# Performance work log

Hardware: AMD Instinct MI355X
Metric: run time of the kernel (lower is better)

The kernel has to match this reference:

```python
import jax, jax.numpy as jnp
import numpy as np

BLOCKS = 32
BLOCK_SIZE = 8
CONV_SHAPES = [(128, 96), (128, 128), (96, 128)] * 2  # per-block conv (out,in) list


def build_conv_meta():
    meta = []
    w_total = 0
    b_total = 0
    for _ in range(BLOCKS):
        for oc, ic in CONV_SHAPES:
            meta.append((oc, ic, w_total, b_total))
            w_total += oc * ic * 9
            b_total += oc
    return meta, w_total, b_total

CONV_META, W_TOTAL, B_TOTAL = build_conv_meta()


def build_program():
    ops = [[0, 0, 0, 0], [1, 0, 0, 0], [2, 0, 0, 0]]
    for blk in range(BLOCKS):
        ops.append([3, 0, 1, 2])  # SPLIT r0 -> (r1, r2)
        for rnd in range(2):
            ci = blk * 6 + rnd * 3
            ops += [
                [4, 3, 2, ci],      # r3 = conv(r2)        128<-96
                [5, 3, 3, 0],       # r3 = relu(r3)
                [4, 3, 3, ci + 1],  # r3 = conv(r3)        128<-128
                [5, 3, 3, 0],       # r3 = relu(r3)
                [4, 3, 3, ci + 2],  # r3 = conv(r3)        96<-128
                [6, 1, 1, 3],       # r1 = r1 + r3
                [9, 1, 2, 0],       # swap(r1, r2)  (Feistel)
            ]
        ops += [[7, 0, 1, 2],       # r0 = concat(r1, r2)
                [8, 0, 0, blk]]     # r0 = mix[blk] @ r0 (1x1 conv)
    return np.array(ops, dtype=np.int64)


def space_to_depth(x, blk):
    b, c, h, w = x.shape
    x = x.reshape(b, c, h // blk, blk, w // blk, blk)
    x = jnp.transpose(x, (0, 1, 3, 5, 2, 4))
    return x.reshape(b, c * blk * blk, h // blk, w // blk)


def conv3x3(x, w, b):
    y = jax.lax.conv_general_dilated(
        x, w, window_strides=(1, 1), padding=[(1, 1), (1, 1)],
        dimension_numbers=('NCHW', 'OIHW', 'NCHW'))
    return y + b[None, :, None, None]


def run_program(x, mu, sigma, w_flat, b_flat, m, perm, ops):
    regs = [x, None, None, None, None]
    for row in np.asarray(ops):
        op, a, b, c = (int(v) for v in row)
        if op == 0:  # AFFINE
            regs[a] = (regs[a] - mu[None, :, None, None]) / sigma[None, :, None, None]
        elif op == 1:  # PERM: gather along flattened HW per channel
            bs, ch, h, w = regs[a].shape
            v = regs[a].reshape(bs, ch, h * w)
            regs[a] = jnp.take_along_axis(v, perm[None], axis=2).reshape(bs, ch, h, w)
        elif op == 2:  # S2D
            regs[a] = space_to_depth(regs[a], BLOCK_SIZE)
        elif op == 3:  # SPLIT
            regs[b], regs[c] = jnp.split(regs[a], 2, axis=1)
        elif op == 4:  # CONV (weights sliced from flat buffer, static offsets)
            oc, ic, woff, boff = CONV_META[c]
            w = w_flat[woff:woff + oc * ic * 9].reshape(oc, ic, 3, 3)
            bb = b_flat[boff:boff + oc]
            regs[a] = conv3x3(regs[b], w, bb)
        elif op == 5:  # RELU
            regs[a] = jax.nn.relu(regs[b])
        elif op == 6:  # ADD
            regs[a] = regs[b] + regs[c]
        elif op == 7:  # CONCAT
            regs[a] = jnp.concatenate([regs[b], regs[c]], axis=1)
        elif op == 8:  # MIX: 1x1 conv with 192x192 orthogonal matrix
            regs[a] = jnp.einsum('oc,bchw->bohw', m[c], regs[b])
        elif op == 9:  # SWAP
            regs[a], regs[b] = regs[b], regs[a]
        else:
            raise ValueError('bad op')
    return regs[0]


def setup_inputs() -> dict:
    key = jax.random.key(0)
    k_x, k_w, k_b = jax.random.split(key, 3)
    rng = np.random.default_rng(0)

    x = jax.random.normal(k_x, (8, 3, 256, 256), dtype=jnp.float32)
    mu = jnp.full((3,), 0.45, dtype=jnp.float32)
    sigma = jnp.full((3,), 0.2, dtype=jnp.float32)
    # conv weights ~ He-ish scale so activations stay bounded across 64 Feistel rounds
    w_flat = jax.random.normal(k_w, (W_TOTAL,), dtype=jnp.float32) * 0.04
    b_flat = jax.random.normal(k_b, (B_TOTAL,), dtype=jnp.float32) * 0.01
    # orthogonal 192x192 mix matrices per block (as in nn.init.orthogonal_)
    ms = []
    for _ in range(BLOCKS):
        q, r = np.linalg.qr(rng.standard_normal((192, 192)))
        q = q * np.sign(np.diag(r))[None, :]
        ms.append(q.astype(np.float32))
    m = jnp.asarray(np.stack(ms))  # [BLOCKS,192,192]
    # per-channel spatial permutation on the 256x256 input
    perm = jnp.asarray(np.stack([rng.permutation(256 * 256) for _ in range(3)]).astype(np.int32))
    ops = build_program()  # static numpy tape
    return {'x': x, 'mu': mu, 'sigma': sigma, 'w_flat': w_flat, 'b_flat': b_flat,
            'm': m, 'perm': perm, 'ops': ops}


def reference(x, mu, sigma, w_flat, b_flat, m, perm, ops):
    return run_program(x, mu, sigma, w_flat, b_flat, m, perm, ops)
```

## Files before the change

### kernel.cpp

```cpp
#include <hip/hip_runtime.h>

typedef _Float16 f16;
typedef _Float16 f16x8 __attribute__((ext_vector_type(8)));
typedef _Float16 f16x4 __attribute__((ext_vector_type(4)));
typedef float    f32x4 __attribute__((ext_vector_type(4)));

#define TPB 256

__global__ __launch_bounds__(TPB) void prologue_k(
    const float* __restrict__ x, const float* __restrict__ mu,
    const float* __restrict__ sigma, const int* __restrict__ perm,
    f16* __restrict__ A0)
{
    int gid = blockIdx.x * TPB + threadIdx.x;
    if (gid >= 8192 * 192) return;
    int c = gid % 192;
    int p = gid / 192;
    int b  = p >> 10;
    int h2 = (p >> 5) & 31;
    int w2 = p & 31;
    int cc = c >> 6;
    int bh = (c >> 3) & 7;
    int bw = c & 7;
    int j   = (h2 * 8 + bh) * 256 + (w2 * 8 + bw);
    int src = perm[cc * 65536 + j];
    float v = (x[(b * 3 + cc) * 65536 + src] - mu[cc]) / sigma[cc];
    A0[gid] = (f16)v;
}

__global__ __launch_bounds__(TPB) void wconv_k(const float* __restrict__ wf,
                                               f16* __restrict__ wh)
{
    int c   = blockIdx.y;
    int idx = blockIdx.x * TPB + threadIdx.x;
    int s   = c % 6;
    int s3  = s % 3;
    int oc  = (s3 == 2) ? 96 : 128;
    int ic  = (s3 == 0) ? 96 : 128;
    int wo  = (s3 == 0 ? 0 : (s3 == 1 ? 110592 : 258048)) + (s >= 3 ? 368640 : 0);
    int ocic = oc * ic;
    int n    = ocic * 9;
    if (idx >= n) return;
    size_t base = (size_t)(c / 6) * 737280 + wo;
    int tap = idx / ocic;
    int r   = idx - tap * ocic;
    int o   = r / ic;
    int i   = r - o * ic;
    wh[base + idx] = (f16)wf[base + (size_t)o * ic * 9 + (size_t)i * 9 + tap];
}

__global__ __launch_bounds__(TPB) void mconv_k(const float* __restrict__ mf,
                                               f16* __restrict__ mh, int n)
{
    int i = blockIdx.x * TPB + threadIdx.x;
    if (i < n) mh[i] = (f16)mf[i];
}

__global__ __launch_bounds__(TPB) void bconv_k(const float* __restrict__ bf,
                                               float* __restrict__ bs, int n)
{
    int i = blockIdx.x * TPB + threadIdx.x;
    if (i < n) bs[i] = ldexpf(bf[i], -(i / 704));
}

template<int IC, int OC, int TAPS, bool RELU, bool ACCUM, bool OUT32>
__global__ __launch_bounds__(TPB) void conv_k(
    const f16* __restrict__ Xin, int ICS,
    const f16* __restrict__ W,  const float* __restrict__ bias,
    f16* __restrict__ Out, int OCS, float* __restrict__ Out32, float scale)
{
    constexpr int R    = 4;
    constexpr int NC8  = IC / 8;
    constexpr int PAD  = (TAPS == 9) ? 1 : 0;
    constexpr int ROWS = R + 2 * PAD;
    constexpr int WW   = 32 + 2 * PAD;

    extern __shared__ f16 lds[];
    f16* Alds = lds + ROWS * NC8 * WW * 8;

    const int tid  = threadIdx.x;
    const int tile = blockIdx.x;
    const int img  = tile >> 3;
    const int r0   = (tile & 7) * R;
    const int oc0  = blockIdx.y * 32;

    for (int i = tid; i < ROWS * WW * NC8; i += TPB) {
        int c8  = i % NC8;
        int rem = i / NC8;
        int wv  = rem % WW;
        int ri  = rem / WW;
        int row = r0 - PAD + ri;
        int wc  = wv - PAD;
        f16x8 v = {};
        if ((unsigned)row < 32u && (unsigned)wc < 32u) {
            int p = img * 1024 + row * 32 + wc;
            v = *(const f16x8*)&Xin[(size_t)p * ICS + c8 * 8];
        }
        *(f16x8*)&lds[((ri * NC8 + c8) * WW + wv) * 8] = v;
    }

    const int lane = tid & 63;
    const int wave = tid >> 6;
    const int lq   = lane >> 4;
    const int ln   = lane & 15;

    f32x4 acc[2][2] = {};

    for (int tap = 0; tap < TAPS; ++tap) {
        __syncthreads();
        for (int i = tid; i < 32 * NC8; i += TPB) {
            int o  = i & 31;
            int c8 = i >> 5;
            *(f16x8*)&Alds[(c8 * 32 + o) * 8] =
                *(const f16x8*)&W[((size_t)tap * OC + oc0 + o) * IC + c8 * 8];
        }
        __syncthreads();

        const int dy = (TAPS == 9) ? tap / 3 - 1 : 0;
        const int dx = (TAPS == 9) ? tap % 3 - 1 : 0;
        const int bb = ((wave + PAD + dy) * NC8 * WW + (ln + dx + PAD)) * 8;

#pragma unroll
        for (int kc = 0; kc < IC / 32; ++kc) {
            f16x8 a0 = *(const f16x8*)&Alds[((kc * 4 + lq) * 32 + ln) * 8];
            f16x8 a1 = *(const f16x8*)&Alds[((kc * 4 + lq) * 32 + 16 + ln) * 8];
            f16x8 b0 = *(const f16x8*)&lds[bb + (kc * 4 + lq) * WW * 8];
            f16x8 b1 = *(const f16x8*)&lds[bb + (kc * 4 + lq) * WW * 8 + 128];
            acc[0][0] = __builtin_amdgcn_mfma_f32_16x16x32_f16(a0, b0, acc[0][0], 0, 0, 0);
            acc[1][0] = __builtin_amdgcn_mfma_f32_16x16x32_f16(a1, b0, acc[1][0], 0, 0, 0);
            acc[0][1] = __builtin_amdgcn_mfma_f32_16x16x32_f16(a0, b1, acc[0][1], 0, 0, 0);
            acc[1][1] = __builtin_amdgcn_mfma_f32_16x16x32_f16(a1, b1, acc[1][1], 0, 0, 0);
        }
    }

    const int prow = r0 + wave;
#pragma unroll
    for (int mm = 0; mm < 2; ++mm) {
#pragma unroll
        for (int nn = 0; nn < 2; ++nn) {
            int oc = oc0 + mm * 16 + lq * 4;
            int p  = img * 1024 + prow * 32 + nn * 16 + ln;
            float b0 = 0.f, b1 = 0.f, b2 = 0.f, b3 = 0.f;
            if (TAPS == 9) {
                float4 bv = *(const float4*)&bias[oc];
                b0 = bv.x; b1 = bv.y; b2 = bv.z; b3 = bv.w;
            }
            float v0 = acc[mm][nn][0] * scale + b0;
            float v1 = acc[mm][nn][1] * scale + b1;
            float v2 = acc[mm][nn][2] * scale + b2;
            float v3 = acc[mm][nn][3] * scale + b3;
            if (RELU) {
                v0 = fmaxf(v0, 0.f); v1 = fmaxf(v1, 0.f);
                v2 = fmaxf(v2, 0.f); v3 = fmaxf(v3, 0.f);
            }
            if (OUT32) {
                size_t ob = (size_t)(img * 192 + oc) * 1024 + prow * 32 + nn * 16 + ln;
                Out32[ob]          = v0;
                Out32[ob + 1024]   = v1;
                Out32[ob + 2048]   = v2;
                Out32[ob + 3072]   = v3;
            } else {
                f16* op = &Out[(size_t)p * OCS + oc];
                if (ACCUM) {
                    f16x4 old = *(const f16x4*)op;
                    v0 += (float)old[0]; v1 += (float)old[1];
                    v2 += (float)old[2]; v3 += (float)old[3];
                }
                f16x4 hv;
                hv[0] = (f16)v0; hv[1] = (f16)v1; hv[2] = (f16)v2; hv[3] = (f16)v3;
                *(f16x4*)op = hv;
            }
        }
    }
}

extern "C" void kernel_launch(void* const* d_in, const int* in_sizes, int n_in,
                              void* d_out, int out_size, void* d_ws, size_t ws_size,
                              hipStream_t stream)
{
    const float* x     = (const float*)d_in[0];
    const float* mu    = (const float*)d_in[1];
    const float* sigma = (const float*)d_in[2];
    const float* wf    = (const float*)d_in[3];
    const float* bf    = (const float*)d_in[4];
    const float* mf    = (const float*)d_in[5];
    const int*   perm  = (const int*)d_in[6];
    float*       out   = (float*)d_out;

    char* ws = (char*)d_ws;
    f16*   WH = (f16*)(ws);
    f16*   MH = (f16*)(ws + 47185920);
    float* BS = (float*)(ws + 49545216);
    f16*   XA = (f16*)(ws + 49635328);
    f16*   XB = (f16*)(ws + 52781056);
    f16*   H1 = (f16*)(ws + 55926784);
    f16*   H2 = (f16*)(ws + 58023936);

    wconv_k<<<dim3(576, 192), TPB, 0, stream>>>(wf, WH);
    mconv_k<<<dim3(4608), TPB, 0, stream>>>(mf, MH, 1179648);
    bconv_k<<<dim3(88),   TPB, 0, stream>>>(bf, BS, 22528);
    prologue_k<<<dim3(6144), TPB, 0, stream>>>(x, mu, sigma, perm, XA);

    static const int wo6[6] = {0, 110592, 258048, 368640, 479232, 626688};
    static const int bo6[6] = {0, 128, 256, 352, 480, 608};

    constexpr int LDS96  = (6 * 12 * 34 * 8 + 96 * 32) * 2;
    constexpr int LDS128 = (6 * 16 * 34 * 8 + 128 * 32) * 2;
    constexpr int LDS192 = (4 * 24 * 32 * 8 + 192 * 32) * 2;

    f16* cur = XA;
    f16* nxt = XB;
    for (int blk = 0; blk < 32; ++blk) {
        int c = blk * 6;
        size_t w0 = (size_t)blk * 737280;
        size_t b0 = (size_t)blk * 704;
        conv_k<96, 128, 9, true,  false, false><<<dim3(64, 4), TPB, LDS96, stream>>>(
            cur + 96, 192, WH + w0 + wo6[0], BS + b0 + bo6[0], H1, 128, nullptr, 1.0f);
        conv_k<128, 128, 9, true,  false, false><<<dim3(64, 4), TPB, LDS128, stream>>>(
            H1, 128, WH + w0 + wo6[1], BS + b0 + bo6[1], H2, 128, nullptr, 1.0f);
        conv_k<128, 96, 9, false, true,  false><<<dim3(64, 3), TPB, LDS128, stream>>>(
            H2, 128, WH + w0 + wo6[2], BS + b0 + bo6[2], cur, 192, nullptr, 1.0f);
        conv_k<96, 128, 9, true,  false, false><<<dim3(64, 4), TPB, LDS96, stream>>>(
            cur, 192, WH + w0 + wo6[3], BS + b0 + bo6[3], H1, 128, nullptr, 1.0f);
        conv_k<128, 128, 9, true,  false, false><<<dim3(64, 4), TPB, LDS128, stream>>>(
            H1, 128, WH + w0 + wo6[4], BS + b0 + bo6[4], H2, 128, nullptr, 1.0f);
        conv_k<128, 96, 9, false, true,  false><<<dim3(64, 3), TPB, LDS128, stream>>>(
            H2, 128, WH + w0 + wo6[5], BS + b0 + bo6[5], cur + 96, 192, nullptr, 1.0f);
        if (blk < 31) {
            conv_k<192, 192, 1, false, false, false><<<dim3(64, 6), TPB, LDS192, stream>>>(
                cur, 192, MH + (size_t)blk * 36864, nullptr, nxt, 192, nullptr, 0.5f);
        } else {
            conv_k<192, 192, 1, false, false, true><<<dim3(64, 6), TPB, LDS192, stream>>>(
                cur, 192, MH + (size_t)blk * 36864, nullptr, nullptr, 192, out,
                2147483648.0f );
        }
        f16* t = cur; cur = nxt; nxt = t;
    }
}
```

Measured before the change: 3.036 ms.

## Replace per-layer launches with persistent kernel using per-image spin barriers

After: 3.718 ms. 1.22x slower.

```diff
diff --git a/kernel.cpp b/kernel.cpp
--- a/kernel.cpp
+++ b/kernel.cpp
@@ -32,21 +32,24 @@
                                                f16* __restrict__ wh)
 {
     int c   = blockIdx.y;
-    int idx = blockIdx.x * TPB + threadIdx.x;
     int s   = c % 6;
     int s3  = s % 3;
-    int oc  = (s3 == 2) ? 96 : 128;
     int ic  = (s3 == 0) ? 96 : 128;
+    int ocv = (s3 == 2) ? 96 : 128;
     int wo  = (s3 == 0 ? 0 : (s3 == 1 ? 110592 : 258048)) + (s >= 3 ? 368640 : 0);
-    int ocic = oc * ic;
-    int n    = ocic * 9;
+    int n   = ocv * ic;
+    int idx = blockIdx.x * TPB + threadIdx.x;
     if (idx >= n) return;
+    int o, i;
+    if (ic == 128) { o = idx >> 7; i = idx & 127; }
+    else           { o = idx / 96; i = idx - o * 96; }
     size_t base = (size_t)(c / 6) * 737280 + wo;
-    int tap = idx / ocic;
-    int r   = idx - tap * ocic;
-    int o   = r / ic;
-    int i   = r - o * ic;
-    wh[base + idx] = (f16)wf[base + (size_t)o * ic * 9 + (size_t)i * 9 + tap];
+    const float* src = &wf[base + ((size_t)o * ic + i) * 9];
+    float v[9];
+#pragma unroll
+    for (int t = 0; t < 9; ++t) v[t] = src[t];
+#pragma unroll
+    for (int t = 0; t < 9; ++t) wh[base + (size_t)t * n + idx] = (f16)v[t];
 }
 
 __global__ __launch_bounds__(TPB) void mconv_k(const float* __restrict__ mf,
@@ -63,114 +66,190 @@
     if (i < n) bs[i] = ldexpf(bf[i], -(i / 704));
 }
 
+__device__ __forceinline__ void img_barrier(unsigned* __restrict__ bar, int img,
+                                            unsigned target)
+{
+    __syncthreads();
+    if (threadIdx.x == 0) {
+        __builtin_amdgcn_fence(__ATOMIC_RELEASE, "agent");
+        __hip_atomic_fetch_add(&bar[img * 32], 1u, __ATOMIC_RELAXED,
+                               __HIP_MEMORY_SCOPE_AGENT);
+        while (__hip_atomic_load(&bar[img * 32], __ATOMIC_RELAXED,
+                                 __HIP_MEMORY_SCOPE_AGENT) < target)
+            __builtin_amdgcn_s_sleep(1);
+        __builtin_amdgcn_fence(__ATOMIC_ACQUIRE, "agent");
+    }
+    __syncthreads();
+}
+
 template<int IC, int OC, int TAPS, bool RELU, bool ACCUM, bool OUT32>
-__global__ __launch_bounds__(TPB) void conv_k(
+__device__ void conv_layer(f16* lds, int img, int local,
     const f16* __restrict__ Xin, int ICS,
-    const f16* __restrict__ W,  const float* __restrict__ bias,
+    const f16* __restrict__ W, const float* __restrict__ bias,
     f16* __restrict__ Out, int OCS, float* __restrict__ Out32, float scale)
 {
-    constexpr int R    = 4;
-    constexpr int NC8  = IC / 8;
-    constexpr int PAD  = (TAPS == 9) ? 1 : 0;
-    constexpr int ROWS = R + 2 * PAD;
-    constexpr int WW   = 32 + 2 * PAD;
-
+    constexpr int NC8   = IC / 8;
+    constexpr int PAD   = (TAPS == 9) ? 1 : 0;
+    constexpr int ROWS  = 4 + 2 * PAD;
+    constexpr int WW    = 32 + 2 * PAD;
+    constexpr int UNITS = 8 * (OC / 32);
+    constexpr int CNT   = 32 * NC8;
+
+    f16* Alds = lds + ROWS * NC8 * WW * 8;
+    const int tid  = threadIdx.x;
+    const int r0   = (local & 7) * 4;
+    const int lane = tid & 63, wave = tid >> 6, lq = lane >> 4, ln = lane & 15;
+
+    for (int rnd = 0; rnd < ((UNITS > 32) ? 2 : 1); ++rnd) {
+        const int u = local + rnd * 32;
+        if (u >= UNITS) break;
+        const int oc0 = (u >> 3) * 32;
+
+        if (rnd == 0) {
+            for (int i = tid; i < ROWS * WW * NC8; i += TPB) {
+                int c8  = i % NC8;
+                int rem = i / NC8;
+                int wv  = rem % WW;
+                int ri  = rem / WW;
+                int row = r0 - PAD + ri;
+                int wc  = wv - PAD;
+                f16x8 v = {};
+                if ((unsigned)row < 32u && (unsigned)wc < 32u) {
+                    int p = img * 1024 + row * 32 + wc;
+                    v = *(const f16x8*)&Xin[(size_t)p * ICS + c8 * 8];
+                }
+                *(f16x8*)&lds[((ri * NC8 + c8) * WW + wv) * 8] = v;
+            }
+        } else {
+            __syncthreads();
+        }
+        for (int i = tid; i < CNT; i += TPB) {
+            int o = i & 31, c8 = i >> 5;
+            *(f16x8*)&Alds[(c8 * 32 + o) * 8] =
+                *(const f16x8*)&W[((size_t)oc0 + o) * IC + c8 * 8];
+        }
+        __syncthreads();
+
+        f32x4 acc[2][2] = {};
+        for (int tap = 0; tap < TAPS; ++tap) {
+            f16x8 w0v = {}, w1v = {};
+            if (TAPS == 9 && tap + 1 < TAPS) {
+                const f16* Wn = &W[((size_t)(tap + 1) * OC + oc0) * IC];
+                { int i = tid;
+                  w0v = *(const f16x8*)&Wn[(size_t)(i & 31) * IC + (i >> 5) * 8]; }
+                if (CNT > 256) { int i = tid + 256; if (i < CNT)
+                  w1v = *(const f16x8*)&Wn[(size_t)(i & 31) * IC + (i >> 5) * 8]; }
+            }
+            const int dy = (TAPS == 9) ? tap / 3 - 1 : 0;
+            const int dx = (TAPS == 9) ? tap % 3 - 1 : 0;
+            const int bb = ((wave + PAD + dy) * NC8 * WW + (ln + dx + PAD)) * 8;
+#pragma unroll
+            for (int kc = 0; kc < IC / 32; ++kc) {
+                f16x8 a0 = *(const f16x8*)&Alds[((kc * 4 + lq) * 32 + ln) * 8];
+                f16x8 a1 = *(const f16x8*)&Alds[((kc * 4 + lq) * 32 + 16 + ln) * 8];
+                f16x8 b0 = *(const f16x8*)&lds[bb + (kc * 4 + lq) * WW * 8];
+                f16x8 b1 = *(const f16x8*)&lds[bb + (kc * 4 + lq) * WW * 8 + 128];
+                acc[0][0] = __builtin_amdgcn_mfma_f32_16x16x32_f16(a0, b0, acc[0][0], 0, 0, 0);
+                acc[1][0] = __builtin_amdgcn_mfma_f32_16x16x32_f16(a1, b0, acc[1][0], 0, 0, 0);
+                acc[0][1] = __builtin_amdgcn_mfma_f32_16x16x32_f16(a0, b1, acc[0][1], 0, 0, 0);
+                acc[1][1] = __builtin_amdgcn_mfma_f32_16x16x32_f16(a1, b1, acc[1][1], 0, 0, 0);
+            }
+            if (TAPS == 9 && tap + 1 < TAPS) {
+                __syncthreads();
+                { int i = tid;
+                  *(f16x8*)&Alds[((i >> 5) * 32 + (i & 31)) * 8] = w0v; }
+                if (CNT > 256) { int i = tid + 256; if (i < CNT)
+                  *(f16x8*)&Alds[((i >> 5) * 32 + (i & 31)) * 8] = w1v; }
+                __syncthreads();
+            }
+        }
+
+        const int prow = r0 + wave;
+#pragma unroll
+        for (int mm = 0; mm < 2; ++mm) {
+#pragma unroll
+            for (int nn = 0; nn < 2; ++nn) {
+                int oc = oc0 + mm * 16 + lq * 4;
+                int p  = img * 1024 + prow * 32 + nn * 16 + ln;
+                float b0 = 0.f, b1 = 0.f, b2 = 0.f, b3 = 0.f;
+                if (TAPS == 9) {
+                    float4 bv = *(const float4*)&bias[oc];
+                    b0 = bv.x; b1 = bv.y; b2 = bv.z; b3 = bv.w;
+                }
+                float v0 = acc[mm][nn][0] * scale + b0;
+                float v1 = acc[mm][nn][1] * scale + b1;
+                float v2 = acc[mm][nn][2] * scale + b2;
+                float v3 = acc[mm][nn][3] * scale + b3;
+                if (RELU) {
+                    v0 = fmaxf(v0, 0.f); v1 = fmaxf(v1, 0.f);
+                    v2 = fmaxf(v2, 0.f); v3 = fmaxf(v3, 0.f);
+                }
+                if (OUT32) {
+                    size_t ob = (size_t)(img * 192 + oc) * 1024 + prow * 32 + nn * 16 + ln;
+                    Out32[ob]        = v0;
+                    Out32[ob + 1024] = v1;
+                    Out32[ob + 2048] = v2;
+                    Out32[ob + 3072] = v3;
+                } else {
+                    f16* op = &Out[(size_t)p * OCS + oc];
+                    if (ACCUM) {
+                        f16x4 old = *(const f16x4*)op;
+                        v0 += (float)old[0]; v1 += (float)old[1];
+                        v2 += (float)old[2]; v3 += (float)old[3];
+                    }
+                    f16x4 hv;
+                    hv[0] = (f16)v0; hv[1] = (f16)v1; hv[2] = (f16)v2; hv[3] = (f16)v3;
+                    *(f16x4*)op = hv;
+                }
+            }
+        }
+    }
+}
+
+__global__ __launch_bounds__(TPB) void persist_k(
+    const f16* __restrict__ WH, const f16* __restrict__ MH,
+    const float* __restrict__ BS, f16* __restrict__ XA, f16* __restrict__ XB,
+    f16* __restrict__ H1, f16* __restrict__ H2, float* __restrict__ out,
+    unsigned* __restrict__ bar)
+{
     extern __shared__ f16 lds[];
-    f16* Alds = lds + ROWS * NC8 * WW * 8;
-
-    const int tid  = threadIdx.x;
-    const int tile = blockIdx.x;
-    const int img  = tile >> 3;
-    const int r0   = (tile & 7) * R;
-    const int oc0  = blockIdx.y * 32;
-
-    for (int i = tid; i < ROWS * WW * NC8; i += TPB) {
-        int c8  = i % NC8;
-        int rem = i / NC8;
-        int wv  = rem % WW;
-        int ri  = rem / WW;
-        int row = r0 - PAD + ri;
-        int wc  = wv - PAD;
-        f16x8 v = {};
-        if ((unsigned)row < 32u && (unsigned)wc < 32u) {
-            int p = img * 1024 + row * 32 + wc;
-            v = *(const f16x8*)&Xin[(size_t)p * ICS + c8 * 8];
-        }
-        *(f16x8*)&lds[((ri * NC8 + c8) * WW + wv) * 8] = v;
-    }
-
-    const int lane = tid & 63;
-    const int wave = tid >> 6;
-    const int lq   = lane >> 4;
-    const int ln   = lane & 15;
-
-    f32x4 acc[2][2] = {};
-
-    for (int tap = 0; tap < TAPS; ++tap) {
-        __syncthreads();
-        for (int i = tid; i < 32 * NC8; i += TPB) {
-            int o  = i & 31;
-            int c8 = i >> 5;
-            *(f16x8*)&Alds[(c8 * 32 + o) * 8] =
-                *(const f16x8*)&W[((size_t)tap * OC + oc0 + o) * IC + c8 * 8];
-        }
-        __syncthreads();
-
-        const int dy = (TAPS == 9) ? tap / 3 - 1 : 0;
-        const int dx = (TAPS == 9) ? tap % 3 - 1 : 0;
-        const int bb = ((wave + PAD + dy) * NC8 * WW + (ln + dx + PAD)) * 8;
-
-#pragma unroll
-        for (int kc = 0; kc < IC / 32; ++kc) {
-            f16x8 a0 = *(const f16x8*)&Alds[((kc * 4 + lq) * 32 + ln) * 8];
-            f16x8 a1 = *(const f16x8*)&Alds[((kc * 4 + lq) * 32 + 16 + ln) * 8];
-            f16x8 b0 = *(const f16x8*)&lds[bb + (kc * 4 + lq) * WW * 8];
-            f16x8 b1 = *(const f16x8*)&lds[bb + (kc * 4 + lq) * WW * 8 + 128];
-            acc[0][0] = __builtin_amdgcn_mfma_f32_16x16x32_f16(a0, b0, acc[0][0], 0, 0, 0);
-            acc[1][0] = __builtin_amdgcn_mfma_f32_16x16x32_f16(a1, b0, acc[1][0], 0, 0, 0);
-            acc[0][1] = __builtin_amdgcn_mfma_f32_16x16x32_f16(a0, b1, acc[0][1], 0, 0, 0);
-            acc[1][1] = __builtin_amdgcn_mfma_f32_16x16x32_f16(a1, b1, acc[1][1], 0, 0, 0);
-        }
-    }
-
-    const int prow = r0 + wave;
-#pragma unroll
-    for (int mm = 0; mm < 2; ++mm) {
-#pragma unroll
-        for (int nn = 0; nn < 2; ++nn) {
-            int oc = oc0 + mm * 16 + lq * 4;
-            int p  = img * 1024 + prow * 32 + nn * 16 + ln;
-            float b0 = 0.f, b1 = 0.f, b2 = 0.f, b3 = 0.f;
-            if (TAPS == 9) {
-                float4 bv = *(const float4*)&bias[oc];
-                b0 = bv.x; b1 = bv.y; b2 = bv.z; b3 = bv.w;
-            }
-            float v0 = acc[mm][nn][0] * scale + b0;
-            float v1 = acc[mm][nn][1] * scale + b1;
-            float v2 = acc[mm][nn][2] * scale + b2;
-            float v3 = acc[mm][nn][3] * scale + b3;
-            if (RELU) {
-                v0 = fmaxf(v0, 0.f); v1 = fmaxf(v1, 0.f);
-                v2 = fmaxf(v2, 0.f); v3 = fmaxf(v3, 0.f);
-            }
-            if (OUT32) {
-                size_t ob = (size_t)(img * 192 + oc) * 1024 + prow * 32 + nn * 16 + ln;
-                Out32[ob]          = v0;
-                Out32[ob + 1024]   = v1;
-                Out32[ob + 2048]   = v2;
-                Out32[ob + 3072]   = v3;
-            } else {
-                f16* op = &Out[(size_t)p * OCS + oc];
-                if (ACCUM) {
-                    f16x4 old = *(const f16x4*)op;
-                    v0 += (float)old[0]; v1 += (float)old[1];
-                    v2 += (float)old[2]; v3 += (float)old[3];
-                }
-                f16x4 hv;
-                hv[0] = (f16)v0; hv[1] = (f16)v1; hv[2] = (f16)v2; hv[3] = (f16)v3;
-                *(f16x4*)op = hv;
-            }
-        }
+    const int wg    = blockIdx.x;
+    const int img   = wg & 7;
+    const int local = wg >> 3;
+    unsigned gen = 0;
+
+    for (int blk = 0; blk < 32; ++blk) {
+        const size_t w0 = (size_t)blk * 737280;
+        const size_t b0 = (size_t)blk * 704;
+        f16* cur = (blk & 1) ? XB : XA;
+        f16* nxt = (blk & 1) ? XA : XB;
+
+        conv_layer<96, 128, 9, true, false, false>(lds, img, local, cur + 96, 192,
+            WH + w0 + 0,      BS + b0 + 0,   H1, 128, nullptr, 1.f);
+        img_barrier(bar, img, ++gen * 32u);
+        conv_layer<128, 128, 9, true, false, false>(lds, img, local, H1, 128,
+            WH + w0 + 110592, BS + b0 + 128, H2, 128, nullptr, 1.f);
+        img_barrier(bar, img, ++gen * 32u);
+        conv_layer<128, 96, 9, false, true, false>(lds, img, local, H2, 128,
+            WH + w0 + 258048, BS + b0 + 256, cur, 192, nullptr, 1.f);
+        img_barrier(bar, img, ++gen * 32u);
+        conv_layer<96, 128, 9, true, false, false>(lds, img, local, cur, 192,
+            WH + w0 + 368640, BS + b0 + 352, H1, 128, nullptr, 1.f);
+        img_barrier(bar, img, ++gen * 32u);
+        conv_layer<128, 128, 9, true, false, false>(lds, img, local, H1, 128,
+            WH + w0 + 479232, BS + b0 + 480, H2, 128, nullptr, 1.f);
+        img_barrier(bar, img, ++gen * 32u);
+        conv_layer<128, 96, 9, false, true, false>(lds, img, local, H2, 128,
+            WH + w0 + 626688, BS + b0 + 608, cur + 96, 192, nullptr, 1.f);
+        img_barrier(bar, img, ++gen * 32u);
+        if (blk < 31)
+            conv_layer<192, 192, 1, false, false, false>(lds, img, local, cur, 192,
+                MH + (size_t)blk * 36864, nullptr, nxt, 192, nullptr, 0.5f);
+        else
+            conv_layer<192, 192, 1, false, false, true>(lds, img, local, cur, 192,
+                MH + (size_t)blk * 36864, nullptr, nullptr, 192, out,
+                2147483648.f );
+        img_barrier(bar, img, ++gen * 32u);
     }
 }
 
@@ -188,52 +267,22 @@
     float*       out   = (float*)d_out;
 
     char* ws = (char*)d_ws;
-    f16*   WH = (f16*)(ws);
-    f16*   MH = (f16*)(ws + 47185920);
-    float* BS = (float*)(ws + 49545216);
-    f16*   XA = (f16*)(ws + 49635328);
-    f16*   XB = (f16*)(ws + 52781056);
-    f16*   H1 = (f16*)(ws + 55926784);
-    f16*   H2 = (f16*)(ws + 58023936);
-
-    wconv_k<<<dim3(576, 192), TPB, 0, stream>>>(wf, WH);
+    f16*      WH  = (f16*)(ws);
+    f16*      MH  = (f16*)(ws + 47185920);
+    float*    BS  = (float*)(ws + 49545216);
+    f16*      XA  = (f16*)(ws + 49635328);
+    f16*      XB  = (f16*)(ws + 52781056);
+    f16*      H1  = (f16*)(ws + 55926784);
+    f16*      H2  = (f16*)(ws + 58023936);
+    unsigned* BAR = (unsigned*)(ws + 60121088);
+
+    hipMemsetAsync(BAR, 0, 4096, stream);
+
+    wconv_k<<<dim3(64, 192), TPB, 0, stream>>>(wf, WH);
     mconv_k<<<dim3(4608), TPB, 0, stream>>>(mf, MH, 1179648);
     bconv_k<<<dim3(88),   TPB, 0, stream>>>(bf, BS, 22528);
     prologue_k<<<dim3(6144), TPB, 0, stream>>>(x, mu, sigma, perm, XA);
 
-    static const int wo6[6] = {0, 110592, 258048, 368640, 479232, 626688};
-    static const int bo6[6] = {0, 128, 256, 352, 480, 608};
-
-    constexpr int LDS96  = (6 * 12 * 34 * 8 + 96 * 32) * 2;
-    constexpr int LDS128 = (6 * 16 * 34 * 8 + 128 * 32) * 2;
-    constexpr int LDS192 = (4 * 24 * 32 * 8 + 192 * 32) * 2;
-
-    f16* cur = XA;
-    f16* nxt = XB;
-    for (int blk = 0; blk < 32; ++blk) {
-        int c = blk * 6;
-        size_t w0 = (size_t)blk * 737280;
-        size_t b0 = (size_t)blk * 704;
-        conv_k<96, 128, 9, true,  false, false><<<dim3(64, 4), TPB, LDS96, stream>>>(
-            cur + 96, 192, WH + w0 + wo6[0], BS + b0 + bo6[0], H1, 128, nullptr, 1.0f);
-        conv_k<128, 128, 9, true,  false, false><<<dim3(64, 4), TPB, LDS128, stream>>>(
-            H1, 128, WH + w0 + wo6[1], BS + b0 + bo6[1], H2, 128, nullptr, 1.0f);
-        conv_k<128, 96, 9, false, true,  false><<<dim3(64, 3), TPB, LDS128, stream>>>(
-            H2, 128, WH + w0 + wo6[2], BS + b0 + bo6[2], cur, 192, nullptr, 1.0f);
-        conv_k<96, 128, 9, true,  false, false><<<dim3(64, 4), TPB, LDS96, stream>>>(
-            cur, 192, WH + w0 + wo6[3], BS + b0 + bo6[3], H1, 128, nullptr, 1.0f);
-        conv_k<128, 128, 9, true,  false, false><<<dim3(64, 4), TPB, LDS128, stream>>>(
-            H1, 128, WH + w0 + wo6[4], BS + b0 + bo6[4], H2, 128, nullptr, 1.0f);
-        conv_k<128, 96, 9, false, true,  false><<<dim3(64, 3), TPB, LDS128, stream>>>(
-            H2, 128, WH + w0 + wo6[5], BS + b0 + bo6[5], cur + 96, 192, nullptr, 1.0f);
-        if (blk < 31) {
-            conv_k<192, 192, 1, false, false, false><<<dim3(64, 6), TPB, LDS192, stream>>>(
-                cur, 192, MH + (size_t)blk * 36864, nullptr, nxt, 192, nullptr, 0.5f);
-        } else {
-            conv_k<192, 192, 1, false, false, true><<<dim3(64, 6), TPB, LDS192, stream>>>(
-                cur, 192, MH + (size_t)blk * 36864, nullptr, nullptr, 192, out,
-                2147483648.0f );
-        }
-        f16* t = cur; cur = nxt; nxt = t;
-    }
-}
+    constexpr int LDSB = 61440;
+    persist_k<<<dim3(256), TPB, LDSB, stream>>>(WH, MH, BS, XA, XB, H1, H2, out, BAR);
+}
```
